# Kernel optimization log

Hardware: AMD Instinct MI355X
Metric: run time of the kernel (lower is better)

Reference implementation:

```python
import jax, jax.numpy as jnp
import numpy as np

LN_EPS = 1e-5


def _act_quant(x):
    # per-token int8 absmax quantization (BitNet style)
    s = 127.0 / jnp.clip(jnp.max(jnp.abs(x), axis=-1, keepdims=True), 1e-5)
    return jnp.clip(jnp.round(x * s), -128.0, 127.0) / s


def _weight_quant(w):
    # ternary 1.58-bit weight quantization with global mean-abs scale
    s = 1.0 / jnp.clip(jnp.mean(jnp.abs(w)), 1e-5)
    return jnp.clip(jnp.round(w * s), -1.0, 1.0) / s


def _ste(x, q):
    # straight-through estimator: forward uses q, gradient flows through x
    return x + jax.lax.stop_gradient(q - x)


def _bitlinear(x, w, b):
    xq = _ste(x, _act_quant(x))
    wq = _ste(w, _weight_quant(w))
    return jnp.einsum('bsd,hd->bsh', xq, wq) + b


def _layernorm(x, gamma, beta):
    mu = jnp.mean(x, axis=-1, keepdims=True)
    var = jnp.mean(jnp.square(x - mu), axis=-1, keepdims=True)
    return (x - mu) * jax.lax.rsqrt(var + LN_EPS) * gamma + beta


def setup_inputs() -> dict:
    key = jax.random.key(0)
    ks = jax.random.split(key, 3)
    B, S, D, H = 4, 4096, 2048, 8192
    return {
        'x': jax.random.normal(ks[0], (B, S, D), dtype=jnp.float32),
        'gamma': jnp.ones((D,), jnp.float32),
        'beta': jnp.zeros((D,), jnp.float32),
        'w1': jax.random.normal(ks[1], (H, D), jnp.float32) * (1.0 / np.sqrt(D)),
        'b1': jnp.zeros((H,), jnp.float32),
        'w2': jax.random.normal(ks[2], (D, H), jnp.float32) * (1.0 / np.sqrt(H)),
        'b2': jnp.zeros((D,), jnp.float32),
    }


def reference(x, gamma, beta, w1, b1, w2, b2):
    h = _layernorm(x, gamma, beta)
    h = _bitlinear(h, w1, b1)            # [B,S,H]
    h = jax.nn.gelu(h, approximate=False)  # torch nn.GELU default = exact erf
    out = _bitlinear(h, w2, b2)          # [B,S,D]
    return out
```

## Files before the change

kernel.cpp:

```cpp
#include <hip/hip_runtime.h>
#include <hip/hip_bf16.h>


typedef __attribute__((ext_vector_type(4))) int int4v;

#define D_DIM 2048
#define H_DIM 8192
#define M_DIM 16384
#define MCHUNK 4096

__device__ __forceinline__ float block_sum(float v, float* buf) {
#pragma unroll
  for (int o = 32; o > 0; o >>= 1) v += __shfl_down(v, o, 64);
  const int lane = threadIdx.x & 63, w = threadIdx.x >> 6;
  if (lane == 0) buf[w] = v;
  __syncthreads();
  float r = buf[0] + buf[1] + buf[2] + buf[3];
  __syncthreads();
  return r;
}
__device__ __forceinline__ float block_max(float v, float* buf) {
#pragma unroll
  for (int o = 32; o > 0; o >>= 1) v = fmaxf(v, __shfl_down(v, o, 64));
  const int lane = threadIdx.x & 63, w = threadIdx.x >> 6;
  if (lane == 0) buf[w] = v;
  __syncthreads();
  float r = fmaxf(fmaxf(buf[0], buf[1]), fmaxf(buf[2], buf[3]));
  __syncthreads();
  return r;
}

__device__ __forceinline__ void lds16(const signed char* g, signed char* l) {
  __builtin_amdgcn_global_load_lds(
      (const __attribute__((address_space(1))) unsigned int*)g,
      (__attribute__((address_space(3))) unsigned int*)l, 16, 0, 0);
}

__global__ __launch_bounds__(256) void absmean_partial2(const float* __restrict__ w1,
                                                        const float* __restrict__ w2,
                                                        int n, double* __restrict__ part1,
                                                        double* __restrict__ part2) {
  __shared__ float buf[4];
  const int half = gridDim.x >> 1;
  const bool second = (int)blockIdx.x >= half;
  const float* w = second ? w2 : w1;
  double* part = second ? part2 : part1;
  const int bid = second ? (blockIdx.x - half) : blockIdx.x;
  float s = 0.0f;
  const long stride = (long)half * 256 * 4;
  for (long i = ((long)bid * 256 + threadIdx.x) * 4; i < n; i += stride) {
    float4 v = *(const float4*)(w + i);
    s += fabsf(v.x) + fabsf(v.y) + fabsf(v.z) + fabsf(v.w);
  }
  float r = block_sum(s, buf);
  if (threadIdx.x == 0) part[bid] = (double)r;
}

__global__ __launch_bounds__(256) void absmean_final2(const double* __restrict__ part1,
                                                      const double* __restrict__ part2,
                                                      int nb, double n,
                                                      double* __restrict__ out) {
  __shared__ double buf[4];
  const double* part = (blockIdx.x == 0) ? part1 : part2;
  double s = 0.0;
  for (int i = threadIdx.x; i < nb; i += 256) s += part[i];
#pragma unroll
  for (int o = 32; o > 0; o >>= 1) s += __shfl_down(s, o, 64);
  const int lane = threadIdx.x & 63, w = threadIdx.x >> 6;
  if (lane == 0) buf[w] = s;
  __syncthreads();
  if (threadIdx.x == 0) out[blockIdx.x] = (buf[0] + buf[1] + buf[2] + buf[3]) / n;
}

__global__ __launch_bounds__(256) void wquant2_kernel(const float* __restrict__ w1,
                                                      const float* __restrict__ w2,
                                                      const double* __restrict__ means,
                                                      signed char* __restrict__ wq1,
                                                      signed char* __restrict__ wq2, int n) {
  const int half = gridDim.x >> 1;
  const bool second = (int)blockIdx.x >= half;
  const float* w = second ? w2 : w1;
  signed char* wq = second ? wq2 : wq1;
  const double mean = second ? means[1] : means[0];
  const int bid = second ? (blockIdx.x - half) : blockIdx.x;
  long i = ((long)bid * 256 + threadIdx.x) * 4;
  if (i >= n) return;
  const float s = 1.0f / (float)fmax(mean, 1e-5);
  float4 v = *(const float4*)(w + i);
  __align__(4) signed char q[4];
  q[0] = (signed char)(int)fminf(fmaxf(rintf(v.x * s), -1.f), 1.f);
  q[1] = (signed char)(int)fminf(fmaxf(rintf(v.y * s), -1.f), 1.f);
  q[2] = (signed char)(int)fminf(fmaxf(rintf(v.z * s), -1.f), 1.f);
  q[3] = (signed char)(int)fminf(fmaxf(rintf(v.w * s), -1.f), 1.f);
  *(int*)(wq + i) = *(int*)q;
}

__global__ __launch_bounds__(256) void ln_quant_kernel(const float* __restrict__ x,
                                                       const float* __restrict__ gamma,
                                                       const float* __restrict__ beta,
                                                       signed char* __restrict__ aq,
                                                       float* __restrict__ ds) {
  __shared__ float buf[4];
  const int t = threadIdx.x;
  const long row = blockIdx.x;
  const float* xr = x + row * (long)D_DIM;
  float v[8];
  *(float4*)(v)     = *(const float4*)(xr + t * 8);
  *(float4*)(v + 4) = *(const float4*)(xr + t * 8 + 4);
  float s = 0.f;
#pragma unroll
  for (int i = 0; i < 8; ++i) s += v[i];
  s = block_sum(s, buf);
  const float mu = s * (1.0f / 2048.0f);
  float sq = 0.f;
#pragma unroll
  for (int i = 0; i < 8; ++i) { float d = v[i] - mu; sq += d * d; }
  sq = block_sum(sq, buf);
  const float inv = 1.0f / sqrtf(sq * (1.0f / 2048.0f) + 1e-5f);
  float gam[8], bet[8];
  *(float4*)(gam)     = *(const float4*)(gamma + t * 8);
  *(float4*)(gam + 4) = *(const float4*)(gamma + t * 8 + 4);
  *(float4*)(bet)     = *(const float4*)(beta + t * 8);
  *(float4*)(bet + 4) = *(const float4*)(beta + t * 8 + 4);
  float xn[8]; float am = 0.f;
#pragma unroll
  for (int i = 0; i < 8; ++i) {
    xn[i] = (v[i] - mu) * inv * gam[i] + bet[i];
    am = fmaxf(am, fabsf(xn[i]));
  }
  am = block_max(am, buf);
  am = fmaxf(am, 1e-5f);
  const float qs = 127.0f / am;
  __align__(8) signed char q[8];
#pragma unroll
  for (int i = 0; i < 8; ++i)
    q[i] = (signed char)(int)fminf(fmaxf(rintf(xn[i] * qs), -128.f), 127.f);
  *(long*)(aq + row * D_DIM + t * 8) = *(long*)q;
  if (t == 0) ds[row] = am / 127.0f;
}

__global__ __launch_bounds__(256) void hquant32_kernel(const float* __restrict__ src,
                                                       signed char* __restrict__ dst,
                                                       float* __restrict__ ds2) {
  __shared__ float buf[4];
  const int t = threadIdx.x;
  const long row = blockIdx.x;
  const float* sr = src + row * (long)H_DIM;
  float v[4][8];
#pragma unroll
  for (int c = 0; c < 4; ++c) {
    *(float4*)(v[c])     = *(const float4*)(sr + (c * 256 + t) * 8);
    *(float4*)(v[c] + 4) = *(const float4*)(sr + (c * 256 + t) * 8 + 4);
  }
  float am = 0.f;
#pragma unroll
  for (int c = 0; c < 4; ++c)
#pragma unroll
    for (int i = 0; i < 8; ++i) am = fmaxf(am, fabsf(v[c][i]));
  am = block_max(am, buf);
  am = fmaxf(am, 1e-5f);
  const float qs = 127.0f / am;
  signed char* dr = dst + row * (long)H_DIM;
#pragma unroll
  for (int c = 0; c < 4; ++c) {
    __align__(8) signed char o[8];
#pragma unroll
    for (int i = 0; i < 8; ++i)
      o[i] = (signed char)(int)fminf(fmaxf(rintf(v[c][i] * qs), -128.f), 127.f);
    *(long*)(dr + (c * 256 + t) * 8) = *(long*)o;
  }
  if (t == 0) ds2[row] = am / 127.0f;
}

__device__ __forceinline__ void read_a2(const signed char* sm, int base, int4v (&af)[2]) {
#pragma unroll
  for (int ms = 0; ms < 2; ++ms)
    af[ms] = *(const int4v*)&sm[base + ms * 1024];
}
__device__ __forceinline__ void read_b4(const signed char* sm, int base, int4v (&bf)[4]) {
#pragma unroll
  for (int ns = 0; ns < 4; ++ns)
    bf[ns] = *(const int4v*)&sm[base + ns * 1024];
}
__device__ __forceinline__ void mfma_half16(const int4v (&af)[2], const int4v (&bf)[4],
                                            int4v (&acc)[4][4], int m0) {
#pragma unroll
  for (int ms = 0; ms < 2; ++ms)
#pragma unroll
    for (int ns = 0; ns < 4; ++ns)
      acc[m0 + ms][ns] = __builtin_amdgcn_mfma_i32_16x16x64_i8(
          af[ms], bf[ns], acc[m0 + ms][ns], 0, 0, 0);
}

template <int EPI>
__global__ __launch_bounds__(512, 4) void gemm256_kernel(
    const signed char* __restrict__ A,
    const signed char* __restrict__ Bm,
    const float* __restrict__ dsA,
    const double* __restrict__ meanw,
    const float* __restrict__ bias,
    float* __restrict__ outf,
    int NBX, int N, int K) {
  __shared__ __align__(16) signed char smA[3 * 256 * 64];
  __shared__ __align__(16) signed char smB[3 * 128 * 64];
  const int tid = threadIdx.x;
  const int lane = tid & 63;
  const int wid = tid >> 6;
  const int wr = wid >> 1;
  const int wcn = wid & 1;

  const int cpx = gridDim.x >> 3;
  const int swz = ((int)blockIdx.x & 7) * cpx + ((int)blockIdx.x >> 3);
  const int bx = swz % NBX, by = swz / NBX;
  const long r0 = (long)by * 256;
  const long c0 = (long)bx * 128;

  const int srow = tid >> 2;
  const int schunk = (tid & 3) ^ (srow & 3) ^ ((srow >> 2) & 3);
  const signed char* gAs = A + (r0 + srow) * (long)K + schunk * 16;
  const signed char* gBs = Bm + (c0 + srow) * (long)K + schunk * 16;

  const int frow = lane & 15;
  const int fchunk = (lane >> 4) ^ (frow & 3) ^ ((frow >> 2) & 3);
  const int fbyte = frow * 64 + fchunk * 16;
  const int baseA = (wr >> 1) * 8192 + (wr & 1) * 4096 + fbyte;
  const int baseB = wcn * 4096 + fbyte;

  int4v acc[4][4] = {};
  int4v afLo[2], afHi[2], bf[4];
  const int nk = K >> 6;

#define STGA(h, t, off)                                                       \
    lds16(gAs + (long)((h) * 128) * K + (long)(t) * 64,                       \
          &smA[(off) + (h) * 8192 + tid * 16]);
#define STGB(t, off)                                                          \
    lds16(gBs + (long)(t) * 64, &smB[(off) + tid * 16]);
#define BAR  __builtin_amdgcn_s_barrier()
#define SCB  __builtin_amdgcn_sched_barrier(0)
#define PRIO1 __builtin_amdgcn_s_setprio(1)
#define PRIO0 __builtin_amdgcn_s_setprio(0)

  STGA(0, 0, 0); STGA(1, 0, 0); STGB(0, 0);
  STGA(0, 1, 16384); STGA(1, 1, 16384); STGB(1, 8192);
  asm volatile("s_waitcnt vmcnt(3)" ::: "memory");
  SCB; BAR; SCB;

  int aC = 0, aN = 16384, aN2 = 32768;
  int bC = 0, bN = 8192, bN2 = 16384;

  for (int t = 0; t < nk; ++t) {
    const bool s = (t + 2 < nk);

    read_a2(smA, aC + baseA, afLo);
    read_b4(smB, bC + baseB, bf);
    read_a2(smA, aC + baseA + 2048, afHi);
    if (s) { STGA(0, t + 2, aN2); STGA(1, t + 2, aN2); STGB(t + 2, bN2); }
    SCB;
    asm volatile("s_waitcnt lgkmcnt(2)" ::: "memory"); SCB;
    PRIO1; mfma_half16(afLo, bf, acc, 0); PRIO0; SCB;
    asm volatile("s_waitcnt lgkmcnt(0)" ::: "memory"); SCB;
    PRIO1; mfma_half16(afHi, bf, acc, 2); PRIO0; SCB;
    if (s) { asm volatile("s_waitcnt vmcnt(3)" ::: "memory"); }
    else   { asm volatile("s_waitcnt vmcnt(0)" ::: "memory"); }
    SCB; BAR; SCB;

    int tmp = aC; aC = aN; aN = aN2; aN2 = tmp;
    tmp = bC; bC = bN; bN = bN2; bN2 = tmp;
  }
#undef STGA
#undef STGB
#undef BAR
#undef SCB
#undef PRIO1
#undef PRIO0

  const float sw = (float)fmax(meanw[0], 1e-5);
#pragma unroll
  for (int m = 0; m < 4; ++m) {
#pragma unroll
    for (int j = 0; j < 4; ++j) {
      const long row = r0 + wr * 64 + m * 16 + (lane >> 4) * 4 + j;
      const float sa = dsA[row] * sw;
#pragma unroll
      for (int n = 0; n < 4; ++n) {
        const long col = c0 + wcn * 64 + n * 16 + (lane & 15);
        float v = (float)acc[m][n][j] * sa + bias[col];
        if (EPI == 1) {
          float gl = 0.5f * v * (1.0f + erff(v * 0.70710678118654752f));
          outf[row * (long)N + col] = gl;
        } else {
          outf[row * (long)N + col] = v;
        }
      }
    }
  }
}

extern "C" void kernel_launch(void* const* d_in, const int* in_sizes, int n_in,
                              void* d_out, int out_size, void* d_ws, size_t ws_size,
                              hipStream_t stream) {
  const float* x     = (const float*)d_in[0];
  const float* gamma = (const float*)d_in[1];
  const float* beta  = (const float*)d_in[2];
  const float* w1    = (const float*)d_in[3];
  const float* b1    = (const float*)d_in[4];
  const float* w2    = (const float*)d_in[5];
  const float* b2    = (const float*)d_in[6];

  char* ws = (char*)d_ws;
  double* part1 = (double*)(ws + 0);
  double* part2 = (double*)(ws + 16384);
  double* means = (double*)(ws + 32768);
  float* ds1  = (float*)(ws + 65536);
  float* ds2  = (float*)(ws + 131072);
  signed char* wq1 = (signed char*)(ws + 1048576l);
  signed char* wq2 = (signed char*)(ws + 17825792l);
  signed char* aq  = (signed char*)(ws + 34603008l);
  signed char* hq  = (signed char*)(ws + 68157440l);

  const int NW = 16777216;
  float* hstage = (float*)d_out;

  absmean_partial2<<<4096, 256, 0, stream>>>(w1, w2, NW, part1, part2);
  absmean_final2<<<2, 256, 0, stream>>>(part1, part2, 2048, (double)NW, means);
  wquant2_kernel<<<32768, 256, 0, stream>>>(w1, w2, means, wq1, wq2, NW);
  ln_quant_kernel<<<16384, 256, 0, stream>>>(x, gamma, beta, aq, ds1);

  for (int c = 0; c < 4; ++c) {
    const long r0 = (long)c * MCHUNK;
    gemm256_kernel<1><<<(H_DIM / 128) * (MCHUNK / 256), 512, 0, stream>>>(
        aq + r0 * D_DIM, wq1, ds1 + r0, means + 0, b1, hstage,
        H_DIM / 128, H_DIM, D_DIM);
    hquant32_kernel<<<MCHUNK, 256, 0, stream>>>(
        hstage, hq + r0 * H_DIM, ds2 + r0);
  }

  gemm256_kernel<2><<<(D_DIM / 128) * (M_DIM / 256), 512, 0, stream>>>(
      hq, wq2, ds2, means + 1, b2, (float*)d_out,
      D_DIM / 128, D_DIM, H_DIM);
}
```

Measured before the change: 859.3 us.

## Load B operand directly from global into registers, bypassing LDS staging

Removes the triple-buffered LDS staging for the B (weight) tile. Each wave now loads its B fragments straight from global memory into registers at the start of every K iteration. This cuts LDS capacity and LDS read traffic, which could raise occupancy. In exchange, B is no longer prefetched ahead, so global-load latency sits on the critical path each iteration, and the four wave rows re-fetch the same B data from cache.

```diff
diff --git a/kernel.cpp b/kernel.cpp
--- a/kernel.cpp
+++ b/kernel.cpp
@@ -177,11 +177,6 @@
   for (int ms = 0; ms < 2; ++ms)
     af[ms] = *(const int4v*)&sm[base + ms * 1024];
 }
-__device__ __forceinline__ void read_b4(const signed char* sm, int base, int4v (&bf)[4]) {
-#pragma unroll
-  for (int ns = 0; ns < 4; ++ns)
-    bf[ns] = *(const int4v*)&sm[base + ns * 1024];
-}
 __device__ __forceinline__ void mfma_half16(const int4v (&af)[2], const int4v (&bf)[4],
                                             int4v (&acc)[4][4], int m0) {
 #pragma unroll
@@ -202,7 +197,6 @@
     float* __restrict__ outf,
     int NBX, int N, int K) {
   __shared__ __align__(16) signed char smA[3 * 256 * 64];
-  __shared__ __align__(16) signed char smB[3 * 128 * 64];
   const int tid = threadIdx.x;
   const int lane = tid & 63;
   const int wid = tid >> 6;
@@ -218,13 +212,14 @@
   const int srow = tid >> 2;
   const int schunk = (tid & 3) ^ (srow & 3) ^ ((srow >> 2) & 3);
   const signed char* gAs = A + (r0 + srow) * (long)K + schunk * 16;
-  const signed char* gBs = Bm + (c0 + srow) * (long)K + schunk * 16;
 
   const int frow = lane & 15;
   const int fchunk = (lane >> 4) ^ (frow & 3) ^ ((frow >> 2) & 3);
   const int fbyte = frow * 64 + fchunk * 16;
   const int baseA = (wr >> 1) * 8192 + (wr & 1) * 4096 + fbyte;
-  const int baseB = wcn * 4096 + fbyte;
+
+  const signed char* gB = Bm + (c0 + wcn * 64 + frow) * (long)K + (lane >> 4) * 16;
+  const long nsK = 16l * (long)K;
 
   int4v acc[4][4] = {};
   int4v afLo[2], afHi[2], bf[4];
@@ -233,42 +228,44 @@
 #define STGA(h, t, off)                                                       \
     lds16(gAs + (long)((h) * 128) * K + (long)(t) * 64,                       \
           &smA[(off) + (h) * 8192 + tid * 16]);
-#define STGB(t, off)                                                          \
-    lds16(gBs + (long)(t) * 64, &smB[(off) + tid * 16]);
+#define BLOAD(t) {                                                            \
+    bf[0] = *(const int4v*)(gB + (long)(t) * 64);                             \
+    bf[1] = *(const int4v*)(gB + nsK + (long)(t) * 64);                       \
+    bf[2] = *(const int4v*)(gB + 2 * nsK + (long)(t) * 64);                   \
+    bf[3] = *(const int4v*)(gB + 3 * nsK + (long)(t) * 64); }
 #define BAR  __builtin_amdgcn_s_barrier()
 #define SCB  __builtin_amdgcn_sched_barrier(0)
 #define PRIO1 __builtin_amdgcn_s_setprio(1)
 #define PRIO0 __builtin_amdgcn_s_setprio(0)
 
-  STGA(0, 0, 0); STGA(1, 0, 0); STGB(0, 0);
-  STGA(0, 1, 16384); STGA(1, 1, 16384); STGB(1, 8192);
-  asm volatile("s_waitcnt vmcnt(3)" ::: "memory");
+  STGA(0, 0, 0); STGA(1, 0, 0);
+  STGA(0, 1, 16384); STGA(1, 1, 16384);
+  asm volatile("s_waitcnt vmcnt(2)" ::: "memory");
   SCB; BAR; SCB;
 
   int aC = 0, aN = 16384, aN2 = 32768;
-  int bC = 0, bN = 8192, bN2 = 16384;
 
   for (int t = 0; t < nk; ++t) {
     const bool s = (t + 2 < nk);
 
+    BLOAD(t);
+    SCB;
+    if (s) { STGA(0, t + 2, aN2); STGA(1, t + 2, aN2); }
     read_a2(smA, aC + baseA, afLo);
-    read_b4(smB, bC + baseB, bf);
     read_a2(smA, aC + baseA + 2048, afHi);
-    if (s) { STGA(0, t + 2, aN2); STGA(1, t + 2, aN2); STGB(t + 2, bN2); }
     SCB;
     asm volatile("s_waitcnt lgkmcnt(2)" ::: "memory"); SCB;
     PRIO1; mfma_half16(afLo, bf, acc, 0); PRIO0; SCB;
     asm volatile("s_waitcnt lgkmcnt(0)" ::: "memory"); SCB;
     PRIO1; mfma_half16(afHi, bf, acc, 2); PRIO0; SCB;
-    if (s) { asm volatile("s_waitcnt vmcnt(3)" ::: "memory"); }
+    if (s) { asm volatile("s_waitcnt vmcnt(2)" ::: "memory"); }
     else   { asm volatile("s_waitcnt vmcnt(0)" ::: "memory"); }
     SCB; BAR; SCB;
 
-    int tmp = aC; aC = aN; aN = aN2; aN2 = tmp;
-    tmp = bC; bC = bN; bN = bN2; bN2 = tmp;
+    const int tmp = aC; aC = aN; aN = aN2; aN2 = tmp;
   }
 #undef STGA
-#undef STGB
+#undef BLOAD
 #undef BAR
 #undef SCB
 #undef PRIO1
```

Measured after the change: 1.494 ms. +73.9%, slower.
